# Performance work log

Measured on AMD Instinct MI355X. Metric: run time of the kernel, lower is better.

The kernel has to match this reference:

```python
import jax, jax.numpy as jnp
import numpy as np

DIM = 512
HEADS = 16
HEAD_DIM = DIM // HEADS
WH, WW = 7, 7
N = WH * WW
OUP = 512
SCALE = HEAD_DIM ** -0.5
NW = 64  # windows per image (mask leading dim)


def _relative_position_index():
    coords = np.stack(np.meshgrid(np.arange(WH), np.arange(WW), indexing='ij'))  # (2,Wh,Ww)
    flat = coords.reshape(2, -1)                           # (2, N)
    rel = flat[:, :, None] - flat[:, None, :]              # (2, N, N)
    rel = rel.transpose(1, 2, 0).astype(np.int64)          # (N, N, 2)
    rel[:, :, 0] += WH - 1
    rel[:, :, 1] += WW - 1
    rel[:, :, 0] *= 2 * WW - 1
    return jnp.asarray(rel.sum(-1))                        # (N, N) int

REL_IDX = _relative_position_index()


def setup_inputs() -> dict:
    key = jax.random.key(0)
    ks = jax.random.split(key, 8)
    B_ = 4096
    x = jax.random.normal(ks[0], (B_, N, DIM), dtype=jnp.float32)
    mask = jnp.zeros((NW, N, N), dtype=jnp.float32)
    qkv_w = jax.random.normal(ks[1], (3 * DIM, DIM), dtype=jnp.float32) * (DIM ** -0.5)
    qkv_b = jax.random.normal(ks[2], (3 * DIM,), dtype=jnp.float32) * 0.02
    table = jax.random.normal(ks[3], ((2 * WH - 1) * (2 * WW - 1), HEADS), dtype=jnp.float32) * 0.02
    proj_w = jax.random.normal(ks[4], (OUP, DIM), dtype=jnp.float32) * (DIM ** -0.5)
    proj_b = jax.random.normal(ks[5], (OUP,), dtype=jnp.float32) * 0.02
    return {"x": x, "mask": mask, "qkv_w": qkv_w, "qkv_b": qkv_b,
            "table": table, "proj_w": proj_w, "proj_b": proj_b}


def reference(x, mask, qkv_w, qkv_b, table, proj_w, proj_b):
    B_, n, c = x.shape
    qkv = x @ qkv_w.T + qkv_b                               # (B_, N, 3C)
    qkv = qkv.reshape(B_, n, 3, HEADS, HEAD_DIM).transpose(2, 0, 3, 1, 4)
    q, k, v = qkv[0], qkv[1], qkv[2]                        # (B_, H, N, hd)
    q = q * SCALE
    attn = jnp.einsum('bhnd,bhmd->bhnm', q, k)              # (B_, H, N, N)
    bias = table[REL_IDX]                                   # (N, N, H) gather
    attn = attn + bias.transpose(2, 0, 1)[None]             # add rel-pos bias
    nW = mask.shape[0]
    attn = attn.reshape(B_ // nW, nW, HEADS, n, n) + mask[None, :, None]
    attn = attn.reshape(B_, HEADS, n, n)
    attn = jax.nn.softmax(attn, axis=-1)
    out = jnp.einsum('bhnm,bhmd->bhnd', attn, v)            # (B_, H, N, hd)
    out = out.transpose(0, 2, 1, 3).reshape(B_, n, c)
    return out @ proj_w.T + proj_b
```

## Files before the change

kernel.cpp:

```cpp
#include <hip/hip_runtime.h>
#include <hip/hip_bf16.h>
#include <stdint.h>

#define DIMC 512
#define HEADS 16
#define HEAD_DIM 32
#define NTOK 49
#define SCALE 0.17677669529663687f

typedef unsigned short u16;
typedef short bf16x8 __attribute__((ext_vector_type(8)));
typedef float f32x4 __attribute__((ext_vector_type(4)));
typedef u16 u16x4 __attribute__((ext_vector_type(4)));
typedef u16 u16x8 __attribute__((ext_vector_type(8)));

#define MFMA16(a, b, c) __builtin_amdgcn_mfma_f32_16x16x32_bf16((a), (b), (c), 0, 0, 0)

__device__ __forceinline__ u16 f2bf(float f) {
  __hip_bfloat16 h = __float2bfloat16(f);
  u16 u;
  __builtin_memcpy(&u, &h, 2);
  return u;
}

__device__ __forceinline__ void gld16(const void* g, void* l) {
  __builtin_amdgcn_global_load_lds(
      (const __attribute__((address_space(1))) uint32_t*)g,
      (__attribute__((address_space(3))) uint32_t*)l, 16, 0, 0);
}

__global__ void cvt_f32_bf16(const float* __restrict__ in, u16* __restrict__ out, int n) {
  const int stride = gridDim.x * blockDim.x;
  for (int i = blockIdx.x * blockDim.x + threadIdx.x; i * 8 < n; i += stride) {
    const float4 v0 = ((const float4*)(in + i * 8))[0];
    const float4 v1 = ((const float4*)(in + i * 8))[1];
    u16x8 r;
    r[0] = f2bf(v0.x); r[1] = f2bf(v0.y); r[2] = f2bf(v0.z); r[3] = f2bf(v0.w);
    r[4] = f2bf(v1.x); r[5] = f2bf(v1.y); r[6] = f2bf(v1.z); r[7] = f2bf(v1.w);
    *(u16x8*)(out + i * 8) = r;
  }
}

__global__ void biasmask_kernel(const float* __restrict__ table, const float* __restrict__ mask,
                                float* __restrict__ bm) {
  const int wm = blockIdx.x >> 4;
  const int h  = blockIdx.x & 15;
  for (int e = threadIdx.x; e < 4096; e += 256) {
    const int i = e >> 6, j = e & 63;
    float v;
    if (i < NTOK && j < NTOK) {
      const int yi = i / 7, xi = i % 7, yj = j / 7, xj = j % 7;
      const int idx = (yi - yj + 6) * 13 + (xi - xj + 6);
      v = table[idx * HEADS + h] + mask[wm * (NTOK * NTOK) + i * NTOK + j];
    } else {
      v = -1e30f;
    }
    bm[(size_t)blockIdx.x * 4096 + e] = v;
  }
}

template<bool OUT_BF16, bool QKV_SCALE>
__global__ void gemm_bf16(const u16* __restrict__ Ap, const u16* __restrict__ Bp,
                          const float* __restrict__ bias, void* __restrict__ Cp,
                          int M, int N, int K, int nxt) {
  __shared__ u16 As[128 * 64];
  __shared__ u16 Bs[128 * 64];
  const int t = threadIdx.x;
  const int lane = t & 63;
  const int q = gridDim.x >> 3;
  const int lin = blockIdx.x;
  const int l = (lin & 7) * q + (lin >> 3);
  const int bm0 = (l / nxt) * 128;
  const int bn0 = (l % nxt) * 128;
  const int wv = t >> 6, wr = wv >> 1, wc = wv & 1;
  const int lr = lane & 15, lg = lane >> 4;

  f32x4 acc[4][4] = {};

  int soff[4];
#pragma unroll
  for (int k = 0; k < 4; ++k) {
    const int c = t + 256 * k;
    const int row = c >> 3, sub = c & 7;
    soff[k] = ((sub ^ (row & 7)) * 8);
  }

  const int nK = K >> 6;
  for (int kt = 0; kt < nK; ++kt) {
    const int k0 = kt << 6;
    __syncthreads();
#pragma unroll
    for (int k = 0; k < 4; ++k) {
      const int c = t + 256 * k;
      const int row = c >> 3;
      gld16(Ap + (size_t)(bm0 + row) * K + k0 + soff[k], As + c * 8);
      gld16(Bp + (size_t)(bn0 + row) * K + k0 + soff[k], Bs + c * 8);
    }
    __syncthreads();

#pragma unroll
    for (int kk = 0; kk < 2; ++kk) {
      bf16x8 af[4], bfr[4];
#pragma unroll
      for (int i = 0; i < 4; ++i) {
        const int row = wr * 64 + i * 16 + lr;
        af[i] = *(const bf16x8*)&As[row * 64 + ((kk * 4 + lg) ^ (row & 7)) * 8];
      }
#pragma unroll
      for (int j = 0; j < 4; ++j) {
        const int row = wc * 64 + j * 16 + lr;
        bfr[j] = *(const bf16x8*)&Bs[row * 64 + ((kk * 4 + lg) ^ (row & 7)) * 8];
      }
#pragma unroll
      for (int i = 0; i < 4; ++i)
#pragma unroll
        for (int j = 0; j < 4; ++j)
          acc[i][j] = MFMA16(af[i], bfr[j], acc[i][j]);
    }
  }

#pragma unroll
  for (int j = 0; j < 4; ++j) {
    const int col = bn0 + wc * 64 + j * 16 + lr;
    const float bv = bias[col];
    const float sc = (QKV_SCALE && col < DIMC) ? SCALE : 1.0f;
#pragma unroll
    for (int i = 0; i < 4; ++i) {
      const int row0 = bm0 + wr * 64 + i * 16 + lg * 4;
#pragma unroll
      for (int r = 0; r < 4; ++r) {
        const float val = (acc[i][j][r] + bv) * sc;
        if (OUT_BF16)
          ((u16*)Cp)[(size_t)(row0 + r) * N + col] = f2bf(val);
        else
          ((float*)Cp)[(size_t)(row0 + r) * N + col] = val;
      }
    }
  }
}

__global__ void attn_win(const u16* __restrict__ qkv, const float* __restrict__ bmask,
                         u16* __restrict__ aout) {
  __shared__ u16 P[4][64 * 72];
  const int t = threadIdx.x, lane = t & 63, wv = t >> 6;
  const int lr = lane & 15, lg = lane >> 4;
  const int w = blockIdx.x >> 2;
  const int h = ((blockIdx.x & 3) << 2) + wv;
  const size_t base = (size_t)w * NTOK * 1536 + h * HEAD_DIM;

  const bf16x8 zf = {};
  bf16x8 qf[4], kf[4];
#pragma unroll
  for (int i = 0; i < 4; ++i) {
    const int row = i * 16 + lr;
    const size_t roff = base + (size_t)row * 1536 + lg * 8;
    qf[i] = (row < NTOK) ? *(const bf16x8*)&qkv[roff] : zf;
    kf[i] = (row < NTOK) ? *(const bf16x8*)&qkv[roff + DIMC] : zf;
  }

  const f32x4 zc = {};
  f32x4 s[4][4];
#pragma unroll
  for (int i = 0; i < 4; ++i)
#pragma unroll
    for (int j = 0; j < 4; ++j)
      s[i][j] = MFMA16(qf[i], kf[j], zc);

  const float* bmp = bmask + (((size_t)(w & 63) * HEADS + h) << 12);
#pragma unroll
  for (int i = 0; i < 4; ++i)
#pragma unroll
    for (int r = 0; r < 4; ++r) {
      const int ii = i * 16 + lg * 4 + r;
#pragma unroll
      for (int j = 0; j < 4; ++j)
        s[i][j][r] += bmp[ii * 64 + j * 16 + lr];
    }

#pragma unroll
  for (int i = 0; i < 4; ++i)
#pragma unroll
    for (int r = 0; r < 4; ++r) {
      float m = fmaxf(fmaxf(s[i][0][r], s[i][1][r]), fmaxf(s[i][2][r], s[i][3][r]));
      m = fmaxf(m, __shfl_xor(m, 1));
      m = fmaxf(m, __shfl_xor(m, 2));
      m = fmaxf(m, __shfl_xor(m, 4));
      m = fmaxf(m, __shfl_xor(m, 8));
      float sum = 0.f;
#pragma unroll
      for (int j = 0; j < 4; ++j) {
        const float e = __expf(s[i][j][r] - m);
        s[i][j][r] = e;
        sum += e;
      }
      sum += __shfl_xor(sum, 1);
      sum += __shfl_xor(sum, 2);
      sum += __shfl_xor(sum, 4);
      sum += __shfl_xor(sum, 8);
      const float rinv = __builtin_amdgcn_rcpf(sum);
#pragma unroll
      for (int j = 0; j < 4; ++j) s[i][j][r] *= rinv;
    }

  u16* Pw = &P[wv][0];
#pragma unroll
  for (int i = 0; i < 4; ++i)
#pragma unroll
    for (int r = 0; r < 4; ++r) {
      const int ii = i * 16 + lg * 4 + r;
#pragma unroll
      for (int j = 0; j < 4; ++j)
        Pw[ii * 72 + j * 16 + lr] = f2bf(s[i][j][r]);
    }

  f32x4 o[4][2] = {};
#pragma unroll
  for (int ks = 0; ks < 2; ++ks) {
    bf16x8 vf[2];
#pragma unroll
    for (int dn = 0; dn < 2; ++dn) {
#pragma unroll
      for (int e = 0; e < 8; ++e) {
        int kk = ks * 32 + lg * 8 + e;
        kk = kk < NTOK ? kk : 0;
        vf[dn][e] = (short)qkv[base + 2 * DIMC + (size_t)kk * 1536 + dn * 16 + lr];
      }
    }
#pragma unroll
    for (int i = 0; i < 4; ++i) {
      const bf16x8 pa = *(const bf16x8*)&Pw[(i * 16 + lr) * 72 + ks * 32 + lg * 8];
#pragma unroll
      for (int dn = 0; dn < 2; ++dn)
        o[i][dn] = MFMA16(pa, vf[dn], o[i][dn]);
    }
  }

#pragma unroll
  for (int i = 0; i < 4; ++i)
#pragma unroll
    for (int r = 0; r < 4; ++r) {
      const int row = i * 16 + lg * 4 + r;
      if (row < NTOK) {
        const size_t ob = ((size_t)w * NTOK + row) * DIMC + h * HEAD_DIM;
#pragma unroll
        for (int dn = 0; dn < 2; ++dn)
          aout[ob + dn * 16 + lr] = f2bf(o[i][dn][r]);
      }
    }
}

extern "C" void kernel_launch(void* const* d_in, const int* in_sizes, int n_in,
                              void* d_out, int out_size, void* d_ws, size_t ws_size,
                              hipStream_t stream) {
  const float* x      = (const float*)d_in[0];
  const float* mask   = (const float*)d_in[1];
  const float* qkv_w  = (const float*)d_in[2];
  const float* qkv_b  = (const float*)d_in[3];
  const float* table  = (const float*)d_in[4];
  const float* proj_w = (const float*)d_in[5];
  const float* proj_b = (const float*)d_in[6];
  float* out = (float*)d_out;

  const int M = 4096 * NTOK;

  char* ws = (char*)d_ws;
  u16*   qkv_bf   = (u16*)ws;
  u16*   wqkv_bf  = (u16*)(ws + 616562688ull);
  u16*   wproj_bf = (u16*)(ws + 618135552ull);
  float* biasmask = (float*)(ws + 618659840ull);
  u16*   x_bf     = (u16*)(ws + 635437056ull);
  u16*   attn_bf  = x_bf;

  cvt_f32_bf16<<<768, 256, 0, stream>>>(qkv_w, wqkv_bf, 1536 * 512);
  cvt_f32_bf16<<<256, 256, 0, stream>>>(proj_w, wproj_bf, 512 * 512);
  biasmask_kernel<<<1024, 256, 0, stream>>>(table, mask, biasmask);
  cvt_f32_bf16<<<1792, 256, 0, stream>>>(x, x_bf, M * DIMC);

  gemm_bf16<true, true><<<1568 * 12, 256, 0, stream>>>(
      x_bf, wqkv_bf, qkv_b, qkv_bf, M, 1536, 512, 12);

  attn_win<<<4096 * 4, 256, 0, stream>>>(qkv_bf, biasmask, attn_bf);

  gemm_bf16<false, false><<<1568 * 4, 256, 0, stream>>>(
      attn_bf, wproj_bf, proj_b, out, M, 512, 512, 4);
}
```

Before: 1.012 ms.

## Double-buffer 256x256 GEMM tiles and stage V through LDS in attention

Replaces the 128x128 single-buffered GEMM with a 512-thread, 256x256-tile kernel. It double-buffers LDS with a new swizzle, prefetches the next K-slice while MFMAs run, and raises wave priority around the MFMA blocks. The window attention kernel now loads V with vectorized coalesced reads into LDS instead of scalar strided global loads, and XOR-swizzles the P buffer in place of padding. This targets global-load latency and uncoalesced V access, at the cost of more registers and LDS per block, which lowers occupancy.

Result: slower. 1.131 ms (+11.7%).

```diff
diff --git a/kernel.cpp b/kernel.cpp
--- a/kernel.cpp
+++ b/kernel.cpp
@@ -11,7 +11,6 @@
 typedef unsigned short u16;
 typedef short bf16x8 __attribute__((ext_vector_type(8)));
 typedef float f32x4 __attribute__((ext_vector_type(4)));
-typedef u16 u16x4 __attribute__((ext_vector_type(4)));
 typedef u16 u16x8 __attribute__((ext_vector_type(8)));
 
 #define MFMA16(a, b, c) __builtin_amdgcn_mfma_f32_16x16x32_bf16((a), (b), (c), 0, 0, 0)
@@ -59,77 +58,113 @@
   }
 }
 
+__device__ __forceinline__ int swz_addr(int row, int col) {
+  return (row >> 1) * 64 + (((((row & 1) << 2) | (col >> 3)) ^ ((row >> 1) & 7)) << 3) + (col & 7);
+}
+
 template<bool OUT_BF16, bool QKV_SCALE>
-__global__ void gemm_bf16(const u16* __restrict__ Ap, const u16* __restrict__ Bp,
-                          const float* __restrict__ bias, void* __restrict__ Cp,
-                          int M, int N, int K, int nxt) {
-  __shared__ u16 As[128 * 64];
-  __shared__ u16 Bs[128 * 64];
+__launch_bounds__(512, 2)
+__global__ void gemm8(const u16* __restrict__ Ap, const u16* __restrict__ Bp,
+                      const float* __restrict__ bias, void* __restrict__ Cp,
+                      int M, int N, int K, int nxt) {
+  __shared__ u16 As[2][8192];
+  __shared__ u16 Bs[2][8192];
   const int t = threadIdx.x;
   const int lane = t & 63;
+  const int wv = t >> 6;
+  const int wr = wv >> 2;
+  const int wc = wv & 3;
+  const int lr = lane & 15, lg = lane >> 4;
+
   const int q = gridDim.x >> 3;
-  const int lin = blockIdx.x;
-  const int l = (lin & 7) * q + (lin >> 3);
-  const int bm0 = (l / nxt) * 128;
-  const int bn0 = (l % nxt) * 128;
-  const int wv = t >> 6, wr = wv >> 1, wc = wv & 1;
-  const int lr = lane & 15, lg = lane >> 4;
-
-  f32x4 acc[4][4] = {};
-
-  int soff[4];
-#pragma unroll
-  for (int k = 0; k < 4; ++k) {
-    const int c = t + 256 * k;
-    const int row = c >> 3, sub = c & 7;
-    soff[k] = ((sub ^ (row & 7)) * 8);
-  }
-
-  const int nK = K >> 6;
+  const int l = (blockIdx.x & 7) * q + (blockIdx.x >> 3);
+  const int bm0 = (l / nxt) * 256;
+  const int bn0 = (l % nxt) * 256;
+
+  f32x4 acc[8][4] = {};
+
+  const u16* agp[2];
+  const u16* bgp[2];
+  int ldst[2];
+#pragma unroll
+  for (int kc = 0; kc < 2; ++kc) {
+    const int c = t + (kc << 9);
+    const int r2 = c >> 3;
+    const int sub = (c & 7) ^ (r2 & 7);
+    const int row = (r2 << 1) | (sub >> 2);
+    const int col = (sub & 3) << 3;
+    agp[kc] = Ap + (size_t)(bm0 + row) * K + col;
+    bgp[kc] = Bp + (size_t)(bn0 + row) * K + col;
+    ldst[kc] = c * 8;
+  }
+
+#pragma unroll
+  for (int kc = 0; kc < 2; ++kc) {
+    gld16(agp[kc], &As[0][ldst[kc]]);
+    gld16(bgp[kc], &Bs[0][ldst[kc]]);
+    agp[kc] += 32; bgp[kc] += 32;
+  }
+  asm volatile("s_waitcnt vmcnt(0)" ::: "memory");
+  __builtin_amdgcn_s_barrier();
+
+  const int nK = K >> 5;
   for (int kt = 0; kt < nK; ++kt) {
-    const int k0 = kt << 6;
-    __syncthreads();
-#pragma unroll
-    for (int k = 0; k < 4; ++k) {
-      const int c = t + 256 * k;
-      const int row = c >> 3;
-      gld16(Ap + (size_t)(bm0 + row) * K + k0 + soff[k], As + c * 8);
-      gld16(Bp + (size_t)(bn0 + row) * K + k0 + soff[k], Bs + c * 8);
-    }
-    __syncthreads();
-
-#pragma unroll
-    for (int kk = 0; kk < 2; ++kk) {
-      bf16x8 af[4], bfr[4];
-#pragma unroll
-      for (int i = 0; i < 4; ++i) {
-        const int row = wr * 64 + i * 16 + lr;
-        af[i] = *(const bf16x8*)&As[row * 64 + ((kk * 4 + lg) ^ (row & 7)) * 8];
-      }
-#pragma unroll
-      for (int j = 0; j < 4; ++j) {
-        const int row = wc * 64 + j * 16 + lr;
-        bfr[j] = *(const bf16x8*)&Bs[row * 64 + ((kk * 4 + lg) ^ (row & 7)) * 8];
-      }
-#pragma unroll
-      for (int i = 0; i < 4; ++i)
-#pragma unroll
-        for (int j = 0; j < 4; ++j)
-          acc[i][j] = MFMA16(af[i], bfr[j], acc[i][j]);
-    }
-  }
-
-#pragma unroll
-  for (int j = 0; j < 4; ++j) {
-    const int col = bn0 + wc * 64 + j * 16 + lr;
+    const int buf = kt & 1;
+    const u16* Asb = &As[buf][0];
+    const u16* Bsb = &Bs[buf][0];
+
+    bf16x8 bfr[4], af[4];
+#pragma unroll
+    for (int nj = 0; nj < 4; ++nj)
+      bfr[nj] = *(const bf16x8*)&Bsb[swz_addr(wc * 64 + nj * 16 + lr, lg * 8)];
+#pragma unroll
+    for (int mi = 0; mi < 4; ++mi)
+      af[mi] = *(const bf16x8*)&Asb[swz_addr(wr * 128 + mi * 16 + lr, lg * 8)];
+    if (kt + 1 < nK) {
+#pragma unroll
+      for (int kc = 0; kc < 2; ++kc) {
+        gld16(agp[kc], &As[buf ^ 1][ldst[kc]]);
+        gld16(bgp[kc], &Bs[buf ^ 1][ldst[kc]]);
+        agp[kc] += 32; bgp[kc] += 32;
+      }
+    }
+    __builtin_amdgcn_s_barrier();
+    __builtin_amdgcn_s_setprio(1);
+#pragma unroll
+    for (int mi = 0; mi < 4; ++mi)
+#pragma unroll
+      for (int nj = 0; nj < 4; ++nj)
+        acc[mi][nj] = MFMA16(af[mi], bfr[nj], acc[mi][nj]);
+    __builtin_amdgcn_s_setprio(0);
+    __builtin_amdgcn_s_barrier();
+
+    bf16x8 af2[4];
+#pragma unroll
+    for (int mi = 0; mi < 4; ++mi)
+      af2[mi] = *(const bf16x8*)&Asb[swz_addr(wr * 128 + (mi + 4) * 16 + lr, lg * 8)];
+    __builtin_amdgcn_s_barrier();
+    __builtin_amdgcn_s_setprio(1);
+#pragma unroll
+    for (int mi = 0; mi < 4; ++mi)
+#pragma unroll
+      for (int nj = 0; nj < 4; ++nj)
+        acc[mi + 4][nj] = MFMA16(af2[mi], bfr[nj], acc[mi + 4][nj]);
+    __builtin_amdgcn_s_setprio(0);
+    if (kt + 1 < nK) asm volatile("s_waitcnt vmcnt(0)" ::: "memory");
+    __builtin_amdgcn_s_barrier();
+  }
+
+#pragma unroll
+  for (int nj = 0; nj < 4; ++nj) {
+    const int col = bn0 + wc * 64 + nj * 16 + lr;
     const float bv = bias[col];
     const float sc = (QKV_SCALE && col < DIMC) ? SCALE : 1.0f;
 #pragma unroll
-    for (int i = 0; i < 4; ++i) {
-      const int row0 = bm0 + wr * 64 + i * 16 + lg * 4;
+    for (int mi = 0; mi < 8; ++mi) {
+      const int row0 = bm0 + wr * 128 + mi * 16 + lg * 4;
 #pragma unroll
       for (int r = 0; r < 4; ++r) {
-        const float val = (acc[i][j][r] + bv) * sc;
+        const float val = (acc[mi][nj][r] + bv) * sc;
         if (OUT_BF16)
           ((u16*)Cp)[(size_t)(row0 + r) * N + col] = f2bf(val);
         else
@@ -141,7 +176,8 @@
 
 __global__ void attn_win(const u16* __restrict__ qkv, const float* __restrict__ bmask,
                          u16* __restrict__ aout) {
-  __shared__ u16 P[4][64 * 72];
+  __shared__ u16 P[4][64 * 64];
+  __shared__ u16 Vs[4][64 * 40];
   const int t = threadIdx.x, lane = t & 63, wv = t >> 6;
   const int lr = lane & 15, lg = lane >> 4;
   const int w = blockIdx.x >> 2;
@@ -158,13 +194,33 @@
     kf[i] = (row < NTOK) ? *(const bf16x8*)&qkv[roff + DIMC] : zf;
   }
 
+  u16x8 vreg[4];
+  const u16x8 vz = {};
+#pragma unroll
+  for (int it = 0; it < 4; ++it) {
+    const int k = it * 16 + (lane >> 2);
+    const int seg = lane & 3;
+    vreg[it] = (k < NTOK) ? *(const u16x8*)&qkv[base + 2 * DIMC + (size_t)k * 1536 + seg * 8]
+                          : vz;
+  }
+
   const f32x4 zc = {};
   f32x4 s[4][4];
+  __builtin_amdgcn_s_setprio(1);
 #pragma unroll
   for (int i = 0; i < 4; ++i)
 #pragma unroll
     for (int j = 0; j < 4; ++j)
       s[i][j] = MFMA16(qf[i], kf[j], zc);
+  __builtin_amdgcn_s_setprio(0);
+
+  u16* Vsw = &Vs[wv][0];
+#pragma unroll
+  for (int it = 0; it < 4; ++it) {
+    const int k = it * 16 + (lane >> 2);
+    const int seg = lane & 3;
+    *(u16x8*)&Vsw[k * 40 + seg * 8] = vreg[it];
+  }
 
   const float* bmp = bmask + (((size_t)(w & 63) * HEADS + h) << 12);
 #pragma unroll
@@ -209,8 +265,10 @@
     for (int r = 0; r < 4; ++r) {
       const int ii = i * 16 + lg * 4 + r;
 #pragma unroll
-      for (int j = 0; j < 4; ++j)
-        Pw[ii * 72 + j * 16 + lr] = f2bf(s[i][j][r]);
+      for (int j = 0; j < 4; ++j) {
+        const int jj = j * 16 + lr;
+        Pw[ii * 64 + (((jj >> 3) ^ (ii & 7)) << 3) + (jj & 7)] = f2bf(s[i][j][r]);
+      }
     }
 
   f32x4 o[4][2] = {};
@@ -221,18 +279,20 @@
     for (int dn = 0; dn < 2; ++dn) {
 #pragma unroll
       for (int e = 0; e < 8; ++e) {
-        int kk = ks * 32 + lg * 8 + e;
-        kk = kk < NTOK ? kk : 0;
-        vf[dn][e] = (short)qkv[base + 2 * DIMC + (size_t)kk * 1536 + dn * 16 + lr];
-      }
-    }
+        const int kk = ks * 32 + lg * 8 + e;
+        vf[dn][e] = (short)Vsw[kk * 40 + dn * 16 + lr];
+      }
+    }
+    __builtin_amdgcn_s_setprio(1);
 #pragma unroll
     for (int i = 0; i < 4; ++i) {
-      const bf16x8 pa = *(const bf16x8*)&Pw[(i * 16 + lr) * 72 + ks * 32 + lg * 8];
+      const int row = i * 16 + lr;
+      const bf16x8 pa = *(const bf16x8*)&Pw[row * 64 + (((ks * 4 + lg) ^ (row & 7)) << 3)];
 #pragma unroll
       for (int dn = 0; dn < 2; ++dn)
         o[i][dn] = MFMA16(pa, vf[dn], o[i][dn]);
     }
+    __builtin_amdgcn_s_setprio(0);
   }
 
 #pragma unroll
@@ -276,11 +336,11 @@
   biasmask_kernel<<<1024, 256, 0, stream>>>(table, mask, biasmask);
   cvt_f32_bf16<<<1792, 256, 0, stream>>>(x, x_bf, M * DIMC);
 
-  gemm_bf16<true, true><<<1568 * 12, 256, 0, stream>>>(
-      x_bf, wqkv_bf, qkv_b, qkv_bf, M, 1536, 512, 12);
+  gemm8<true, true><<<784 * 6, 512, 0, stream>>>(
+      x_bf, wqkv_bf, qkv_b, qkv_bf, M, 1536, 512, 6);
 
   attn_win<<<4096 * 4, 256, 0, stream>>>(qkv_bf, biasmask, attn_bf);
 
-  gemm_bf16<false, false><<<1568 * 4, 256, 0, stream>>>(
-      attn_bf, wproj_bf, proj_b, out, M, 512, 512, 4);
-}
+  gemm8<false, false><<<784 * 2, 512, 0, stream>>>(
+      attn_bf, wproj_bf, proj_b, out, M, 512, 512, 2);
+}
```

## Fuse x conversion into QKV GEMM and streamline window attention softmax

Applied to the files above, without the earlier changes.

Drops the standalone f32-to-bf16 pass over x by converting A tiles on the fly inside the QKV GEMM. The attention kernel now preloads bias+mask in MFMA fragment layout as the accumulator init and stages V through LDS with vector loads. It also skips the row-max subtraction and computes softmax denominators with an MFMA against a ones vector. Costs: heavier synchronous f32 loads in the GEMM, reread per column tile, and no overflow protection in exp.

Result: slower. 1.188 ms (+17.4%).

```diff
diff --git a/kernel.cpp b/kernel.cpp
--- a/kernel.cpp
+++ b/kernel.cpp
@@ -11,7 +11,6 @@
 typedef unsigned short u16;
 typedef short bf16x8 __attribute__((ext_vector_type(8)));
 typedef float f32x4 __attribute__((ext_vector_type(4)));
-typedef u16 u16x4 __attribute__((ext_vector_type(4)));
 typedef u16 u16x8 __attribute__((ext_vector_type(8)));
 
 #define MFMA16(a, b, c) __builtin_amdgcn_mfma_f32_16x16x32_bf16((a), (b), (c), 0, 0, 0)
@@ -46,12 +45,14 @@
   const int wm = blockIdx.x >> 4;
   const int h  = blockIdx.x & 15;
   for (int e = threadIdx.x; e < 4096; e += 256) {
-    const int i = e >> 6, j = e & 63;
+    const int r = e & 3, lane = (e >> 2) & 63, fj = (e >> 8) & 3, fi = e >> 10;
+    const int row = fi * 16 + (lane >> 4) * 4 + r;
+    const int col = fj * 16 + (lane & 15);
     float v;
-    if (i < NTOK && j < NTOK) {
-      const int yi = i / 7, xi = i % 7, yj = j / 7, xj = j % 7;
+    if (row < NTOK && col < NTOK) {
+      const int yi = row / 7, xi = row % 7, yj = col / 7, xj = col % 7;
       const int idx = (yi - yj + 6) * 13 + (xi - xj + 6);
-      v = table[idx * HEADS + h] + mask[wm * (NTOK * NTOK) + i * NTOK + j];
+      v = table[idx * HEADS + h] + mask[wm * (NTOK * NTOK) + row * NTOK + col];
     } else {
       v = -1e30f;
     }
@@ -59,17 +60,16 @@
   }
 }
 
-template<bool OUT_BF16, bool QKV_SCALE>
-__global__ void gemm_bf16(const u16* __restrict__ Ap, const u16* __restrict__ Bp,
-                          const float* __restrict__ bias, void* __restrict__ Cp,
-                          int M, int N, int K, int nxt) {
+template<bool A_F32, bool OUT_BF16, bool QKV_SCALE>
+__global__ void gemm_tn(const void* __restrict__ Ap, const u16* __restrict__ Bp,
+                        const float* __restrict__ bias, void* __restrict__ Cp,
+                        int M, int N, int K, int nxt) {
   __shared__ u16 As[128 * 64];
   __shared__ u16 Bs[128 * 64];
   const int t = threadIdx.x;
   const int lane = t & 63;
   const int q = gridDim.x >> 3;
-  const int lin = blockIdx.x;
-  const int l = (lin & 7) * q + (lin >> 3);
+  const int l = (blockIdx.x & 7) * q + (blockIdx.x >> 3);
   const int bm0 = (l / nxt) * 128;
   const int bn0 = (l % nxt) * 128;
   const int wv = t >> 6, wr = wv >> 1, wc = wv & 1;
@@ -85,6 +85,9 @@
     soff[k] = ((sub ^ (row & 7)) * 8);
   }
 
+  const int arow = t >> 1;
+  const int acb  = (t & 1) * 32;
+
   const int nK = K >> 6;
   for (int kt = 0; kt < nK; ++kt) {
     const int k0 = kt << 6;
@@ -93,8 +96,27 @@
     for (int k = 0; k < 4; ++k) {
       const int c = t + 256 * k;
       const int row = c >> 3;
-      gld16(Ap + (size_t)(bm0 + row) * K + k0 + soff[k], As + c * 8);
       gld16(Bp + (size_t)(bn0 + row) * K + k0 + soff[k], Bs + c * 8);
+      if (!A_F32)
+        gld16((const u16*)Ap + (size_t)(bm0 + row) * K + k0 + soff[k], As + c * 8);
+    }
+    if (A_F32) {
+      const float* A = (const float*)Ap;
+      const float* src = A + (size_t)(bm0 + arow) * K + k0 + acb;
+      float4 v[8];
+#pragma unroll
+      for (int c = 0; c < 8; ++c) v[c] = ((const float4*)src)[c];
+      u16* dst = &As[arow * 64];
+#pragma unroll
+      for (int cc = 0; cc < 4; ++cc) {
+        bf16x8 p;
+        p[0] = f2bf(v[2 * cc].x); p[1] = f2bf(v[2 * cc].y);
+        p[2] = f2bf(v[2 * cc].z); p[3] = f2bf(v[2 * cc].w);
+        p[4] = f2bf(v[2 * cc + 1].x); p[5] = f2bf(v[2 * cc + 1].y);
+        p[6] = f2bf(v[2 * cc + 1].z); p[7] = f2bf(v[2 * cc + 1].w);
+        const int chunk = (acb >> 3) + cc;
+        *(bf16x8*)&dst[(chunk ^ (arow & 7)) << 3] = p;
+      }
     }
     __syncthreads();
 
@@ -104,12 +126,12 @@
 #pragma unroll
       for (int i = 0; i < 4; ++i) {
         const int row = wr * 64 + i * 16 + lr;
-        af[i] = *(const bf16x8*)&As[row * 64 + ((kk * 4 + lg) ^ (row & 7)) * 8];
+        af[i] = *(const bf16x8*)&As[row * 64 + (((kk * 4 + lg) ^ (row & 7)) << 3)];
       }
 #pragma unroll
       for (int j = 0; j < 4; ++j) {
         const int row = wc * 64 + j * 16 + lr;
-        bfr[j] = *(const bf16x8*)&Bs[row * 64 + ((kk * 4 + lg) ^ (row & 7)) * 8];
+        bfr[j] = *(const bf16x8*)&Bs[row * 64 + (((kk * 4 + lg) ^ (row & 7)) << 3)];
       }
 #pragma unroll
       for (int i = 0; i < 4; ++i)
@@ -139,15 +161,24 @@
   }
 }
 
-__global__ void attn_win(const u16* __restrict__ qkv, const float* __restrict__ bmask,
+__global__ void attn_win(const u16* __restrict__ qkv, const float* __restrict__ bmfrag,
                          u16* __restrict__ aout) {
-  __shared__ u16 P[4][64 * 72];
+  __shared__ u16 P[4][64 * 64];
+  __shared__ u16 Vs[4][64 * 40];
   const int t = threadIdx.x, lane = t & 63, wv = t >> 6;
   const int lr = lane & 15, lg = lane >> 4;
   const int w = blockIdx.x >> 2;
   const int h = ((blockIdx.x & 3) << 2) + wv;
   const size_t base = (size_t)w * NTOK * 1536 + h * HEAD_DIM;
 
+  const float* bmp = bmfrag + (((size_t)(w & 63) * 16 + h) << 12);
+  f32x4 s[4][4];
+#pragma unroll
+  for (int i = 0; i < 4; ++i)
+#pragma unroll
+    for (int j = 0; j < 4; ++j)
+      s[i][j] = *(const f32x4*)&bmp[((i * 4 + j) * 64 + lane) * 4];
+
   const bf16x8 zf = {};
   bf16x8 qf[4], kf[4];
 #pragma unroll
@@ -158,62 +189,50 @@
     kf[i] = (row < NTOK) ? *(const bf16x8*)&qkv[roff + DIMC] : zf;
   }
 
-  const f32x4 zc = {};
-  f32x4 s[4][4];
+  u16x8 vreg[4];
+  const u16x8 vz = {};
+#pragma unroll
+  for (int it = 0; it < 4; ++it) {
+    const int k = it * 16 + (lane >> 2);
+    const int seg = lane & 3;
+    vreg[it] = (k < NTOK) ? *(const u16x8*)&qkv[base + 2 * DIMC + (size_t)k * 1536 + seg * 8]
+                          : vz;
+  }
+
+  __builtin_amdgcn_s_setprio(1);
 #pragma unroll
   for (int i = 0; i < 4; ++i)
 #pragma unroll
     for (int j = 0; j < 4; ++j)
-      s[i][j] = MFMA16(qf[i], kf[j], zc);
-
-  const float* bmp = bmask + (((size_t)(w & 63) * HEADS + h) << 12);
+      s[i][j] = MFMA16(qf[i], kf[j], s[i][j]);
+  __builtin_amdgcn_s_setprio(0);
+
+  u16* Vsw = &Vs[wv][0];
+#pragma unroll
+  for (int it = 0; it < 4; ++it) {
+    const int k = it * 16 + (lane >> 2);
+    const int seg = lane & 3;
+    *(u16x8*)&Vsw[k * 40 + seg * 8] = vreg[it];
+  }
+
+  u16* Pw = &P[wv][0];
 #pragma unroll
   for (int i = 0; i < 4; ++i)
 #pragma unroll
     for (int r = 0; r < 4; ++r) {
       const int ii = i * 16 + lg * 4 + r;
 #pragma unroll
-      for (int j = 0; j < 4; ++j)
-        s[i][j][r] += bmp[ii * 64 + j * 16 + lr];
-    }
-
-#pragma unroll
-  for (int i = 0; i < 4; ++i)
-#pragma unroll
-    for (int r = 0; r < 4; ++r) {
-      float m = fmaxf(fmaxf(s[i][0][r], s[i][1][r]), fmaxf(s[i][2][r], s[i][3][r]));
-      m = fmaxf(m, __shfl_xor(m, 1));
-      m = fmaxf(m, __shfl_xor(m, 2));
-      m = fmaxf(m, __shfl_xor(m, 4));
-      m = fmaxf(m, __shfl_xor(m, 8));
-      float sum = 0.f;
-#pragma unroll
       for (int j = 0; j < 4; ++j) {
-        const float e = __expf(s[i][j][r] - m);
-        s[i][j][r] = e;
-        sum += e;
-      }
-      sum += __shfl_xor(sum, 1);
-      sum += __shfl_xor(sum, 2);
-      sum += __shfl_xor(sum, 4);
-      sum += __shfl_xor(sum, 8);
-      const float rinv = __builtin_amdgcn_rcpf(sum);
-#pragma unroll
-      for (int j = 0; j < 4; ++j) s[i][j][r] *= rinv;
-    }
-
-  u16* Pw = &P[wv][0];
-#pragma unroll
-  for (int i = 0; i < 4; ++i)
-#pragma unroll
-    for (int r = 0; r < 4; ++r) {
-      const int ii = i * 16 + lg * 4 + r;
-#pragma unroll
-      for (int j = 0; j < 4; ++j)
-        Pw[ii * 72 + j * 16 + lr] = f2bf(s[i][j][r]);
-    }
-
+        const int jj = j * 16 + lr;
+        Pw[ii * 64 + (((jj >> 3) ^ (ii & 7)) << 3) + (jj & 7)] = f2bf(__expf(s[i][j][r]));
+      }
+    }
+
+  bf16x8 ones;
+#pragma unroll
+  for (int e = 0; e < 8; ++e) ones[e] = (short)0x3F80;
   f32x4 o[4][2] = {};
+  f32x4 osum[4] = {};
 #pragma unroll
   for (int ks = 0; ks < 2; ++ks) {
     bf16x8 vf[2];
@@ -221,18 +240,21 @@
     for (int dn = 0; dn < 2; ++dn) {
 #pragma unroll
       for (int e = 0; e < 8; ++e) {
-        int kk = ks * 32 + lg * 8 + e;
-        kk = kk < NTOK ? kk : 0;
-        vf[dn][e] = (short)qkv[base + 2 * DIMC + (size_t)kk * 1536 + dn * 16 + lr];
-      }
-    }
+        const int kk = ks * 32 + lg * 8 + e;
+        vf[dn][e] = (short)Vsw[kk * 40 + dn * 16 + lr];
+      }
+    }
+    __builtin_amdgcn_s_setprio(1);
 #pragma unroll
     for (int i = 0; i < 4; ++i) {
-      const bf16x8 pa = *(const bf16x8*)&Pw[(i * 16 + lr) * 72 + ks * 32 + lg * 8];
+      const int row = i * 16 + lr;
+      const bf16x8 pa = *(const bf16x8*)&Pw[row * 64 + (((ks * 4 + lg) ^ (row & 7)) << 3)];
 #pragma unroll
       for (int dn = 0; dn < 2; ++dn)
         o[i][dn] = MFMA16(pa, vf[dn], o[i][dn]);
-    }
+      osum[i] = MFMA16(pa, ones, osum[i]);
+    }
+    __builtin_amdgcn_s_setprio(0);
   }
 
 #pragma unroll
@@ -241,10 +263,11 @@
     for (int r = 0; r < 4; ++r) {
       const int row = i * 16 + lg * 4 + r;
       if (row < NTOK) {
+        const float rinv = __builtin_amdgcn_rcpf(osum[i][r]);
         const size_t ob = ((size_t)w * NTOK + row) * DIMC + h * HEAD_DIM;
 #pragma unroll
         for (int dn = 0; dn < 2; ++dn)
-          aout[ob + dn * 16 + lr] = f2bf(o[i][dn][r]);
+          aout[ob + dn * 16 + lr] = f2bf(o[i][dn][r] * rinv);
       }
     }
 }
@@ -268,19 +291,17 @@
   u16*   wqkv_bf  = (u16*)(ws + 616562688ull);
   u16*   wproj_bf = (u16*)(ws + 618135552ull);
   float* biasmask = (float*)(ws + 618659840ull);
-  u16*   x_bf     = (u16*)(ws + 635437056ull);
-  u16*   attn_bf  = x_bf;
+  u16*   attn_bf  = (u16*)(ws + 635437056ull);
 
   cvt_f32_bf16<<<768, 256, 0, stream>>>(qkv_w, wqkv_bf, 1536 * 512);
   cvt_f32_bf16<<<256, 256, 0, stream>>>(proj_w, wproj_bf, 512 * 512);
   biasmask_kernel<<<1024, 256, 0, stream>>>(table, mask, biasmask);
-  cvt_f32_bf16<<<1792, 256, 0, stream>>>(x, x_bf, M * DIMC);
-
-  gemm_bf16<true, true><<<1568 * 12, 256, 0, stream>>>(
-      x_bf, wqkv_bf, qkv_b, qkv_bf, M, 1536, 512, 12);
+
+  gemm_tn<true, true, true><<<1568 * 12, 256, 0, stream>>>(
+      x, wqkv_bf, qkv_b, qkv_bf, M, 1536, 512, 12);
 
   attn_win<<<4096 * 4, 256, 0, stream>>>(qkv_bf, biasmask, attn_bf);
 
-  gemm_bf16<false, false><<<1568 * 4, 256, 0, stream>>>(
+  gemm_tn<false, false, false><<<1568 * 4, 256, 0, stream>>>(
       attn_bf, wproj_bf, proj_b, out, M, 512, 512, 4);
 }
```
